# Optimization experiments

Hardware: AMD Instinct MI355X
Metric: run time of the kernel (lower is better)

## Reference

```python
import jax, jax.numpy as jnp
import numpy as np

B, T, NMELS = 2, 2048, 64
D, H, DH, M, L = 256, 4, 64, 384, 4
FF2 = 2 * 4 * D  # GLU doubles the 4*dim hidden


def _layernorm(x, g, b):
    m = x.mean(-1, keepdims=True)
    v = ((x - m) ** 2).mean(-1, keepdims=True)
    return (x - m) * jax.lax.rsqrt(v + 1e-5) * g + b


def _conv(h, w, groups=1, pad='VALID'):
    return jax.lax.conv_general_dilated(h, w, (1, 1), pad, feature_group_count=groups,
                                        dimension_numbers=('NCHW', 'OIHW', 'NCHW'))


def _bn(h, g, b, m, v):
    return (h - m[:, None, None]) * jax.lax.rsqrt(v[:, None, None] + 1e-5) * g[:, None, None] + b[:, None, None]


def setup_inputs():
    key = jax.random.key(0)
    ks = jax.random.split(key, 40)
    def n(i, shape, s):
        return (jax.random.normal(ks[i], shape) * s).astype(jnp.float32)
    z = lambda shape: jnp.zeros(shape, jnp.float32)
    o = lambda shape: jnp.ones(shape, jnp.float32)
    return dict(
        x=n(0, (B, T, NMELS), 1.0),
        conv0_w=n(1, (4, 1, 1, 1), 0.5),
        dw1_w=n(2, (4, 1, 3, 3), 0.3), dw1_b=z(4),
        pw1_w=n(3, (D // 2, 4, 1, 1), 0.5), pw1_b=z(D // 2),
        bn1_g=o(D // 2), bn1_b=z(D // 2), bn1_m=n(4, (D // 2,), 0.05), bn1_v=o(D // 2),
        dw2_w=n(5, (D // 2, 1, 3, 3), 0.3), dw2_b=z(D // 2),
        pw2_w=n(6, (D, D // 2, 1, 1), 0.1), pw2_b=z(D),
        bn2_g=o(D), bn2_b=z(D), bn2_m=n(7, (D,), 0.05), bn2_v=o(D),
        proj_w=n(8, (D, D), 0.06), proj_b=z(D),
        ln0_g=o(D), ln0_b=z(D),
        pos_emb=n(9, (1, T, D), 0.02),
        ln1_g=o((L, D)), ln1_b=z((L, D)),
        wq=n(10, (L, D, D), 0.06), bq=z((L, D)),
        wk=n(11, (L, D, D), 0.06), bk=z((L, D)),
        wv=n(12, (L, D, D), 0.06), bv=z((L, D)),
        wo=n(13, (L, D, D), 0.06), bo=z((L, D)),
        proj_mat=n(14, (L, M, DH), 1.0),
        ln2_g=o((L, D)), ln2_b=z((L, D)),
        ffw1=n(15, (L, D, FF2), 0.06), ffb1=z((L, FF2)),
        ffw2=n(16, (L, FF2 // 2, D), 0.03), ffb2=z((L, D)),
        clf_w1=n(17, (D, D // 2), 0.06), clf_b1=z(D // 2),
        clf_ln_g=o(D // 2), clf_ln_b=z(D // 2),
        clf_w2=n(18, (D // 2, 1), 0.09), clf_b2=z(1),
    )


def reference(x, conv0_w, dw1_w, dw1_b, pw1_w, pw1_b, bn1_g, bn1_b, bn1_m, bn1_v,
              dw2_w, dw2_b, pw2_w, pw2_b, bn2_g, bn2_b, bn2_m, bn2_v,
              proj_w, proj_b, ln0_g, ln0_b, pos_emb,
              ln1_g, ln1_b, wq, bq, wk, bk, wv, bv, wo, bo, proj_mat,
              ln2_g, ln2_b, ffw1, ffb1, ffw2, ffb2,
              clf_w1, clf_b1, clf_ln_g, clf_ln_b, clf_w2, clf_b2):
    pad1 = ((1, 1), (1, 1))
    # conv frontend: [B,T,n_mels] -> [B,1,n_mels,T]
    h = x.transpose(0, 2, 1)[:, None]
    h = _conv(h, conv0_w)
    h = _conv(h, dw1_w, groups=4, pad=pad1) + dw1_b[:, None, None]
    h = _conv(h, pw1_w) + pw1_b[:, None, None]
    h = jax.nn.relu(_bn(h, bn1_g, bn1_b, bn1_m, bn1_v))
    h = _conv(h, dw2_w, groups=D // 2, pad=pad1) + dw2_b[:, None, None]
    h = _conv(h, pw2_w) + pw2_b[:, None, None]
    h = jax.nn.relu(_bn(h, bn2_g, bn2_b, bn2_m, bn2_v))
    h = h.mean(axis=2).transpose(0, 2, 1)  # [B,T,D]
    h = h @ proj_w + proj_b
    h = _layernorm(h, ln0_g, ln0_b) + pos_emb[:, :h.shape[1]]
    # reversible Performer: streams x1 (attn) / x2 (ff), combined by sum
    x1, x2 = h, h
    dn = DH ** -0.25
    for l in range(L):
        a = _layernorm(x2, ln1_g[l], ln1_b[l])
        Bsz, N, _ = a.shape
        q = (a @ wq[l] + bq[l]).reshape(Bsz, N, H, DH).transpose(0, 2, 1, 3)
        k = (a @ wk[l] + bk[l]).reshape(Bsz, N, H, DH).transpose(0, 2, 1, 3)
        v = (a @ wv[l] + bv[l]).reshape(Bsz, N, H, DH).transpose(0, 2, 1, 3)
        # FAVOR+ generalized (ReLU) kernel feature maps, eps=1e-3
        qf = jax.nn.relu(jnp.einsum('bhnd,jd->bhnj', dn * q, proj_mat[l])) + 1e-3
        kf = jax.nn.relu(jnp.einsum('bhnd,jd->bhnj', dn * k, proj_mat[l])) + 1e-3
        d_inv = 1.0 / jnp.einsum('bhnj,bhj->bhn', qf, kf.sum(axis=2))
        ctx = jnp.einsum('bhnj,bhnd->bhjd', kf, v)
        o = jnp.einsum('bhjd,bhnj,bhn->bhnd', ctx, qf, d_inv)
        o = o.transpose(0, 2, 1, 3).reshape(Bsz, N, D)
        x1 = x1 + (o @ wo[l] + bo[l])
        f = _layernorm(x1, ln2_g[l], ln2_b[l])
        u1, u2 = jnp.split(f @ ffw1[l] + ffb1[l], 2, axis=-1)
        x2 = x2 + (jax.nn.gelu(u1, approximate=False) * u2) @ ffw2[l] + ffb2[l]
    h = x1 + x2
    c = jax.nn.relu(_layernorm(h @ clf_w1 + clf_b1, clf_ln_g, clf_ln_b))
    return (c @ clf_w2 + clf_b2)[..., 0]
```

## Files before the change

### kernel.cpp

```cpp
#include <hip/hip_runtime.h>
#include <hip/hip_bf16.h>
#include <math.h>

using bf16 = __hip_bfloat16;
typedef __attribute__((ext_vector_type(8))) short short8;
typedef __attribute__((ext_vector_type(4))) float f32x4;

__device__ __forceinline__ float tof(float x) { return x; }
__device__ __forceinline__ float tof(bf16 x) { return __bfloat162float(x); }
__device__ __forceinline__ float b2f(unsigned short u) {
  union { float f; unsigned int i; } c; c.i = ((unsigned int)u) << 16; return c.f;
}
__device__ __forceinline__ unsigned short f2bu(float v) {
  bf16 h = __float2bfloat16(v);
  return *(unsigned short*)&h;
}
__device__ __forceinline__ void sto1(float* p, float v) { *p = v; }
__device__ __forceinline__ void sto1(bf16* p, float v) { *p = __float2bfloat16(v); }

__device__ __forceinline__ float gelu_exact(float x) {
  return 0.5f * x * (1.f + erff(x * 0.70710678118654752f));
}

__device__ __forceinline__ void llds16(const bf16* g, short* l) {
  __builtin_amdgcn_global_load_lds((const __attribute__((address_space(1))) void*)g,
                                   (__attribute__((address_space(3))) void*)l, 16, 0, 0);
}

__global__ __launch_bounds__(256) void pack_qkv_kernel(
    const float* __restrict__ wq, const float* __restrict__ wk,
    const float* __restrict__ wv, bf16* __restrict__ out)
{
  int idx = blockIdx.x * 256 + threadIdx.x;
  int k = idx & 255;
  int nl = idx >> 8;
  int n = nl % 768, l = nl / 768;
  const float* src = (n < 256) ? wq : (n < 512 ? wk : wv);
  out[idx] = __float2bfloat16(src[(long)l * 65536 + k * 256 + (n & 255)]);
}

__global__ __launch_bounds__(256) void pack_qkvbias_kernel(
    const float* __restrict__ bq, const float* __restrict__ bk,
    const float* __restrict__ bv, float* __restrict__ out)
{
  int i = blockIdx.x * 256 + threadIdx.x;
  if (i >= 3072) return;
  int n = i % 768, l = i / 768;
  const float* src = (n < 256) ? bq : (n < 512 ? bk : bv);
  out[i] = src[l * 256 + (n & 255)];
}

__global__ __launch_bounds__(256) void tconv_kernel(
    const float* __restrict__ in, bf16* __restrict__ out,
    int K, int N, long sin, long sout)
{
  int l = blockIdx.z;
  int idx = blockIdx.x * 256 + threadIdx.x;
  int k = idx % K, n = idx / K;
  out[l * sout + idx] = __float2bfloat16(in[l * sin + (long)k * N + n]);
}

__global__ __launch_bounds__(256) void f2b_kernel(
    const float* __restrict__ in, bf16* __restrict__ out, int n)
{
  int i = blockIdx.x * 256 + threadIdx.x;
  if (i < n) out[i] = __float2bfloat16(in[i]);
}

__global__ __launch_bounds__(256) void zero4_kernel(float* __restrict__ p) {
  int i = (blockIdx.x * 256 + threadIdx.x) * 4;
  float4 z; z.x = 0.f; z.y = 0.f; z.z = 0.f; z.w = 0.f;
  *(float4*)&p[i] = z;
}

__global__ __launch_bounds__(256) void sumb_kernel(
    const float* __restrict__ a, const float* __restrict__ b, bf16* __restrict__ o)
{
  int i = (blockIdx.x * 256 + threadIdx.x) * 4;
  float4 x = *(const float4*)&a[i];
  float4 y = *(const float4*)&b[i];
  ushort4 p;
  p.x = f2bu(x.x + y.x); p.y = f2bu(x.y + y.y);
  p.z = f2bu(x.z + y.z); p.w = f2bu(x.w + y.w);
  *(ushort4*)((unsigned short*)o + i) = p;
}

__global__ __launch_bounds__(256) void front1_kernel(
    const float* __restrict__ x, const float* __restrict__ c0w,
    const float* __restrict__ d1w, const float* __restrict__ d1b,
    const float* __restrict__ p1w, const float* __restrict__ p1b,
    const float* __restrict__ g1, const float* __restrict__ b1,
    const float* __restrict__ m1, const float* __restrict__ v1,
    bf16* __restrict__ A1)
{
  __shared__ float sd[256];
  __shared__ float spw[512];
  __shared__ float ss[128], st[128], sb[128];
  int tid = threadIdx.x;
  int bt = blockIdx.x;
  int b = bt >> 11, t = bt & 2047;
  if (tid < 128) {
    float s = g1[tid] * rsqrtf(v1[tid] + 1e-5f);
    ss[tid] = s;
    st[tid] = b1[tid] - m1[tid] * s;
    sb[tid] = p1b[tid];
#pragma unroll
    for (int c = 0; c < 4; ++c) spw[c * 128 + tid] = p1w[tid * 4 + c];
  }
  {
    int c = tid >> 6, f = tid & 63;
    float cw = c0w[c];
    float acc = d1b[c];
#pragma unroll
    for (int kh = 0; kh < 3; ++kh) {
      int fi = f + kh - 1;
      if (fi < 0 || fi >= 64) continue;
#pragma unroll
      for (int kw = 0; kw < 3; ++kw) {
        int ti = t + kw - 1;
        if (ti < 0 || ti >= 2048) continue;
        acc += d1w[c * 9 + kh * 3 + kw] * cw * x[((long)b * 2048 + ti) * 64 + fi];
      }
    }
    sd[c * 64 + f] = acc;
  }
  __syncthreads();
  long ob = (long)bt * 8192;
  for (int it = 0; it < 32; ++it) {
    int o = it * 256 + tid;
    int f = o >> 7, ci = o & 127;
    float pre = sb[ci];
#pragma unroll
    for (int c = 0; c < 4; ++c) pre = fmaf(spw[c * 128 + ci], sd[c * 64 + f], pre);
    A1[ob + o] = __float2bfloat16(fmaxf(fmaf(ss[ci], pre, st[ci]), 0.f));
  }
}

__global__ __launch_bounds__(256, 4) void convtail_kernel(
    const bf16* __restrict__ A1, const float* __restrict__ w,
    const float* __restrict__ wb, const bf16* __restrict__ w2b,
    const float* __restrict__ pb, const float* __restrict__ g2,
    const float* __restrict__ b2, const float* __restrict__ m2,
    const float* __restrict__ v2, bf16* __restrict__ hconvb)
{
  __shared__ short dw2s[64 * 136];
  __shared__ short Bs[64 * 136];
  __shared__ float red[1024];
  __shared__ float ssc[64], ssh[64];
  int tid = threadIdx.x;
  int lane = tid & 63, wv = tid >> 6;
  int quad = lane >> 4, l15 = lane & 15;
  int rw = (wv >> 1) * 32, cw = (wv & 1) * 32;
  int bt = blockIdx.x, b = bt >> 11, t = bt & 2047;
  int ci8 = (tid & 15) * 8;
  float wreg[9][8], breg[8];
#pragma unroll
  for (int c = 0; c < 8; ++c) {
    breg[c] = wb[ci8 + c];
#pragma unroll
    for (int kk = 0; kk < 9; ++kk) wreg[kk][c] = w[(ci8 + c) * 9 + kk];
  }
  const unsigned short* A1u = (const unsigned short*)A1;
  for (int pass = 0; pass < 4; ++pass) {
    int f = pass * 16 + (tid >> 4);
    float a[8];
#pragma unroll
    for (int c = 0; c < 8; ++c) a[c] = breg[c];
#pragma unroll
    for (int kh = 0; kh < 3; ++kh) {
      int fi = f + kh - 1;
      if (fi < 0 || fi >= 64) continue;
#pragma unroll
      for (int kw = 0; kw < 3; ++kw) {
        int ti = t + kw - 1;
        if (ti < 0 || ti >= 2048) continue;
        short8 u = *(const short8*)&A1u[(((long)b * 2048 + ti) * 64 + fi) * 128 + ci8];
        int kk = kh * 3 + kw;
#pragma unroll
        for (int c = 0; c < 8; ++c)
          a[c] = fmaf(wreg[kk][c], b2f((unsigned short)u[c]), a[c]);
      }
    }
    short8 p;
#pragma unroll
    for (int c = 0; c < 8; ++c) p[c] = (short)f2bu(a[c]);
    *(short8*)&dw2s[f * 136 + ci8] = p;
  }
  for (int ct = 0; ct < 4; ++ct) {
    int co0 = ct * 64;
    __syncthreads();
    for (int l2 = 0; l2 < 4; ++l2) {
      int idx = l2 * 256 + tid;
      int row = idx >> 4, koff = (idx & 15) * 8;
      *(short8*)&Bs[row * 136 + koff] =
          *(const short8*)&w2b[(long)(co0 + row) * 128 + koff];
    }
    if (tid < 64) {
      int co = co0 + tid;
      float s = g2[co] * rsqrtf(v2[co] + 1e-5f);
      ssc[tid] = s;
      ssh[tid] = b2[co] - m2[co] * s + s * pb[co];
    }
    __syncthreads();
    f32x4 zv = {0.f, 0.f, 0.f, 0.f};
    f32x4 acc[2][2] = {{zv, zv}, {zv, zv}};
#pragma unroll
    for (int kc = 0; kc < 4; ++kc) {
      short8 a0 = *(const short8*)&dw2s[(rw + l15) * 136 + kc * 32 + quad * 8];
      short8 a1 = *(const short8*)&dw2s[(rw + 16 + l15) * 136 + kc * 32 + quad * 8];
      short8 b0 = *(const short8*)&Bs[(cw + l15) * 136 + kc * 32 + quad * 8];
      short8 b1 = *(const short8*)&Bs[(cw + 16 + l15) * 136 + kc * 32 + quad * 8];
      acc[0][0] = __builtin_amdgcn_mfma_f32_16x16x32_bf16(a0, b0, acc[0][0], 0, 0, 0);
      acc[0][1] = __builtin_amdgcn_mfma_f32_16x16x32_bf16(a0, b1, acc[0][1], 0, 0, 0);
      acc[1][0] = __builtin_amdgcn_mfma_f32_16x16x32_bf16(a1, b0, acc[1][0], 0, 0, 0);
      acc[1][1] = __builtin_amdgcn_mfma_f32_16x16x32_bf16(a1, b1, acc[1][1], 0, 0, 0);
    }
#pragma unroll
    for (int mi = 0; mi < 2; ++mi)
#pragma unroll
      for (int nj = 0; nj < 2; ++nj) {
        int colg = cw + nj * 16 + l15;
        float s = ssc[colg], sh = ssh[colg];
        float sum = 0.f;
#pragma unroll
        for (int r = 0; r < 4; ++r) sum += fmaxf(fmaf(s, acc[mi][nj][r], sh), 0.f);
        int rowgroup = (wv >> 1) * 8 + mi * 4 + quad;
        red[rowgroup * 64 + colg] = sum;
      }
    __syncthreads();
    if (tid < 64) {
      float s = 0.f;
#pragma unroll
      for (int r = 0; r < 16; ++r) s += red[r * 64 + tid];
      hconvb[(long)bt * 256 + co0 + tid] = __float2bfloat16(s * (1.f / 64.f));
    }
  }
}

__global__ __launch_bounds__(256) void favor_kernel(
    const bf16* __restrict__ qkvb, const bf16* __restrict__ pm,
    bf16* __restrict__ qf, bf16* __restrict__ kfT, float dn)
{
  __shared__ short As[4096];
  __shared__ short Bs[4096];
  int tid = threadIdx.x;
  int lane = tid & 63, w = tid >> 6;
  int quad = lane >> 4, l15 = lane & 15;
  int rw = (w >> 1) * 32, cw = (w & 1) * 32;
  int r0 = blockIdx.x * 64, n0 = blockIdx.y * 64;
  int z16 = blockIdx.z;
  bool isK = z16 >= 8;
  int z = z16 & 7, zb = z >> 2, zh = z & 3;
  const bf16* A = qkvb + (isK ? 256 : 0) + (long)zb * 1572864 + zh * 64;
  f32x4 zv = {0.f, 0.f, 0.f, 0.f};
  f32x4 acc[2][2] = {{zv, zv}, {zv, zv}};
  const bf16* Ag = A + (long)(r0 + (tid >> 2)) * 768 + ((tid & 3) * 8);
  const bf16* Bg = pm + (long)(n0 + (tid >> 2)) * 64 + ((tid & 3) * 8);
  llds16(Ag, &As[tid * 8]);
  llds16(Ag + 32, &As[tid * 8 + 2048]);
  llds16(Bg, &Bs[tid * 8]);
  llds16(Bg + 32, &Bs[tid * 8 + 2048]);
  __syncthreads();
#pragma unroll
  for (int c = 0; c < 2; ++c) {
    short8 a0 = *(const short8*)&As[c * 2048 + (rw + l15) * 32 + quad * 8];
    short8 a1 = *(const short8*)&As[c * 2048 + (rw + 16 + l15) * 32 + quad * 8];
    short8 b0 = *(const short8*)&Bs[c * 2048 + (cw + l15) * 32 + quad * 8];
    short8 b1 = *(const short8*)&Bs[c * 2048 + (cw + 16 + l15) * 32 + quad * 8];
    acc[0][0] = __builtin_amdgcn_mfma_f32_16x16x32_bf16(a0, b0, acc[0][0], 0, 0, 0);
    acc[0][1] = __builtin_amdgcn_mfma_f32_16x16x32_bf16(a0, b1, acc[0][1], 0, 0, 0);
    acc[1][0] = __builtin_amdgcn_mfma_f32_16x16x32_bf16(a1, b0, acc[1][0], 0, 0, 0);
    acc[1][1] = __builtin_amdgcn_mfma_f32_16x16x32_bf16(a1, b1, acc[1][1], 0, 0, 0);
  }
  bf16* qfz = qf + (long)zb * 3145728 + (long)zh * 786432;
  unsigned short* kfz = (unsigned short*)kfT + (long)zb * 3145728 + (long)zh * 786432;
#pragma unroll
  for (int mi = 0; mi < 2; ++mi)
#pragma unroll
    for (int nj = 0; nj < 2; ++nj) {
      int colg = n0 + cw + nj * 16 + l15;
      int rbase = r0 + rw + mi * 16 + quad * 4;
      float ov[4];
#pragma unroll
      for (int r = 0; r < 4; ++r)
        ov[r] = fmaxf(acc[mi][nj][r] * dn, 0.f) + 1e-3f;
      if (!isK) {
#pragma unroll
        for (int r = 0; r < 4; ++r)
          qfz[(long)(rbase + r) * 384 + colg] = __float2bfloat16(ov[r]);
      } else {
        ushort4 p;
        p.x = f2bu(ov[0]); p.y = f2bu(ov[1]); p.z = f2bu(ov[2]); p.w = f2bu(ov[3]);
        *(ushort4*)&kfz[(long)colg * 2048 + rbase] = p;
      }
    }
}

__global__ __launch_bounds__(256) void rowsum_kernel(
    const bf16* __restrict__ kfT, float* __restrict__ ksum)
{
  int z = blockIdx.x;
  int j = blockIdx.y * 4 + (threadIdx.x >> 6);
  int lane = threadIdx.x & 63;
  const short* base = (const short*)kfT + ((long)z * 384 + j) * 2048;
  float acc = 0.f;
#pragma unroll
  for (int i = 0; i < 4; ++i) {
    short8 v = *(const short8*)&base[i * 512 + lane * 8];
#pragma unroll
    for (int e = 0; e < 8; ++e) acc += b2f((unsigned short)v[e]);
  }
#pragma unroll
  for (int o = 32; o > 0; o >>= 1) acc += __shfl_xor(acc, o, 64);
  if (lane == 0) ksum[z * 384 + j] = acc;
}

template <typename CTy, int EPI>
__global__ __launch_bounds__(256) void mgemm_kernel(
    const bf16* __restrict__ A, const bf16* __restrict__ Bt,
    const float* __restrict__ bias, const float* __restrict__ res,
    const float* __restrict__ rowsc, CTy* __restrict__ C, bf16* __restrict__ C2,
    int K, int lda, int ldbt, int ldc,
    long sAb, long sAh, long sBb, long sBh, long sCb, long sCh,
    long sRb, long sRh, int Hdiv, float alpha)
{
  __shared__ short As[4096];
  __shared__ short Bs[4096];
  __shared__ short Bs2[(EPI == 8) ? 4096 : 8];
  int tid = threadIdx.x;
  int lane = tid & 63, w = tid >> 6;
  int quad = lane >> 4, l15 = lane & 15;
  int rw = (w >> 1) * 32, cw = (w & 1) * 32;
  int r0 = blockIdx.x * 64, n0 = blockIdx.y * 64;
  int zb = blockIdx.z / Hdiv, zh = blockIdx.z % Hdiv;
  A += zb * sAb + zh * sAh;
  Bt += zb * sBb + zh * sBh;
  C += zb * sCb + zh * sCh;
  if (res) res += zb * sCb + zh * sCh;
  const float* rsp = (EPI == 3) ? rowsc + zb * sRb + zh * sRh : nullptr;
  f32x4 zv = {0.f, 0.f, 0.f, 0.f};
  f32x4 acc[2][2] = {{zv, zv}, {zv, zv}};
  f32x4 acc2[2][2] = {{zv, zv}, {zv, zv}};
  const bf16* Ag = A + (long)(r0 + (tid >> 2)) * lda + ((tid & 3) * 8);
  const bf16* Bg = Bt + (long)(n0 + (tid >> 2)) * ldbt + ((tid & 3) * 8);
  const bf16* Bg2 = (EPI == 8) ? Bg + sRb : nullptr;
  short* Asd = &As[tid * 8];
  short* Bsd = &Bs[tid * 8];
  short* Bs2d = &Bs2[(EPI == 8) ? tid * 8 : 0];
  for (int k0 = 0; k0 < K; k0 += 64) {
    if (k0) __syncthreads();
    llds16(Ag + k0, Asd);
    llds16(Ag + k0 + 32, Asd + 2048);
    llds16(Bg + k0, Bsd);
    llds16(Bg + k0 + 32, Bsd + 2048);
    if constexpr (EPI == 8) {
      llds16(Bg2 + k0, Bs2d);
      llds16(Bg2 + k0 + 32, Bs2d + 2048);
    }
    __syncthreads();
#pragma unroll
    for (int c = 0; c < 2; ++c) {
      short8 a0 = *(const short8*)&As[c * 2048 + (rw + l15) * 32 + quad * 8];
      short8 a1 = *(const short8*)&As[c * 2048 + (rw + 16 + l15) * 32 + quad * 8];
      short8 b0 = *(const short8*)&Bs[c * 2048 + (cw + l15) * 32 + quad * 8];
      short8 b1 = *(const short8*)&Bs[c * 2048 + (cw + 16 + l15) * 32 + quad * 8];
      acc[0][0] = __builtin_amdgcn_mfma_f32_16x16x32_bf16(a0, b0, acc[0][0], 0, 0, 0);
      acc[0][1] = __builtin_amdgcn_mfma_f32_16x16x32_bf16(a0, b1, acc[0][1], 0, 0, 0);
      acc[1][0] = __builtin_amdgcn_mfma_f32_16x16x32_bf16(a1, b0, acc[1][0], 0, 0, 0);
      acc[1][1] = __builtin_amdgcn_mfma_f32_16x16x32_bf16(a1, b1, acc[1][1], 0, 0, 0);
      if constexpr (EPI == 8) {
        short8 c0 = *(const short8*)&Bs2[c * 2048 + (cw + l15) * 32 + quad * 8];
        short8 c1 = *(const short8*)&Bs2[c * 2048 + (cw + 16 + l15) * 32 + quad * 8];
        acc2[0][0] = __builtin_amdgcn_mfma_f32_16x16x32_bf16(a0, c0, acc2[0][0], 0, 0, 0);
        acc2[0][1] = __builtin_amdgcn_mfma_f32_16x16x32_bf16(a0, c1, acc2[0][1], 0, 0, 0);
        acc2[1][0] = __builtin_amdgcn_mfma_f32_16x16x32_bf16(a1, c0, acc2[1][0], 0, 0, 0);
        acc2[1][1] = __builtin_amdgcn_mfma_f32_16x16x32_bf16(a1, c1, acc2[1][1], 0, 0, 0);
      }
    }
  }
#pragma unroll
  for (int mi = 0; mi < 2; ++mi)
#pragma unroll
    for (int nj = 0; nj < 2; ++nj) {
      int colg = n0 + cw + nj * 16 + l15;
      float bv_ = bias ? bias[colg] : 0.f;
      float bv2 = (EPI == 8) ? bias[colg + 1024] : 0.f;
      int rbase = r0 + rw + mi * 16 + quad * 4;
      float ov[4];
#pragma unroll
      for (int r = 0; r < 4; ++r) {
        float v = acc[mi][nj][r];
        if constexpr (EPI == 0 || EPI == 5) {
          v += bv_;
        } else if constexpr (EPI == 1) {
          v += bv_ + res[(long)(rbase + r) * ldc + colg];
        } else if constexpr (EPI == 3) {
          v *= rsp[rbase + r];
        } else if constexpr (EPI == 8) {
          v = gelu_exact(v + bv_) * (acc2[mi][nj][r] + bv2);
        }
        ov[r] = v;
      }
      if constexpr (EPI == 5) {
        if (colg < 512) {
#pragma unroll
          for (int r = 0; r < 4; ++r) sto1(&C[(long)(rbase + r) * ldc + colg], ov[r]);
        } else {
          int bb = rbase >> 11, t0 = rbase & 2047;
          long off = (((long)bb * 4 + ((colg - 512) >> 6)) * 64 + (colg & 63)) * 2048 + t0;
          ushort4 p;
          p.x = f2bu(ov[0]); p.y = f2bu(ov[1]); p.z = f2bu(ov[2]); p.w = f2bu(ov[3]);
          *(ushort4*)((unsigned short*)C2 + off) = p;
        }
      } else if constexpr (EPI == 7) {
#pragma unroll
        for (int r = 0; r < 4; ++r)
          atomicAdd((float*)&C[(long)(rbase + r) * ldc + colg], ov[r]);
      } else {
#pragma unroll
        for (int r = 0; r < 4; ++r) sto1(&C[(long)(rbase + r) * ldc + colg], ov[r]);
      }
    }
  (void)alpha;
}

template <int DIM, bool RELU, bool ADDPOS, bool DUAL, typename OTy>
__global__ __launch_bounds__(256) void ln_kernel(
    const float* __restrict__ in, const float* __restrict__ g,
    const float* __restrict__ b, const float* __restrict__ pos,
    OTy* __restrict__ out0, float* __restrict__ out1)
{
  constexpr int CH = DIM / 64;
  int row = blockIdx.x * 4 + (threadIdx.x >> 6);
  int lane = threadIdx.x & 63;
  const float* rp = in + (long)row * DIM + lane * CH;
  float v[CH];
#pragma unroll
  for (int i = 0; i < CH; ++i) v[i] = rp[i];
  float s = 0.f;
#pragma unroll
  for (int i = 0; i < CH; ++i) s += v[i];
#pragma unroll
  for (int o = 32; o > 0; o >>= 1) s += __shfl_xor(s, o, 64);
  float mean = s * (1.f / DIM);
  float q = 0.f;
#pragma unroll
  for (int i = 0; i < CH; ++i) { float d = v[i] - mean; q += d * d; }
#pragma unroll
  for (int o = 32; o > 0; o >>= 1) q += __shfl_xor(q, o, 64);
  float rstd = rsqrtf(q * (1.f / DIM) + 1e-5f);
  int t = row & 2047;
#pragma unroll
  for (int i = 0; i < CH; ++i) {
    int c = lane * CH + i;
    float o = (v[i] - mean) * rstd * g[c] + b[c];
    if constexpr (ADDPOS) o += pos[(long)t * DIM + c];
    if constexpr (RELU) o = fmaxf(o, 0.f);
    sto1(&out0[(long)row * DIM + c], o);
    if constexpr (DUAL) out1[(long)row * DIM + c] = o;
  }
}

__global__ __launch_bounds__(256) void dinv_kernel(
    const bf16* __restrict__ qf, const float* __restrict__ ksum,
    float* __restrict__ dinv)
{
  int z = blockIdx.x;
  int t = blockIdx.y * 4 + (threadIdx.x >> 6);
  int lane = threadIdx.x & 63;
  const bf16* qr = qf + ((long)z * 2048 + t) * 384;
  const float* ks = ksum + z * 384;
  float acc = 0.f;
#pragma unroll
  for (int i = 0; i < 6; ++i) {
    int j = lane + i * 64;
    acc = fmaf(tof(qr[j]), ks[j], acc);
  }
#pragma unroll
  for (int o = 32; o > 0; o >>= 1) acc += __shfl_xor(acc, o, 64);
  if (lane == 0) dinv[z * 2048 + t] = 1.f / acc;
}

__global__ __launch_bounds__(256) void clf2_kernel(
    const float* __restrict__ c2, const float* __restrict__ w,
    const float* __restrict__ b, float* __restrict__ out)
{
  int row = blockIdx.x * 4 + (threadIdx.x >> 6);
  int lane = threadIdx.x & 63;
  const float* rp = c2 + (long)row * 128 + lane * 2;
  float acc = rp[0] * w[lane * 2] + rp[1] * w[lane * 2 + 1];
#pragma unroll
  for (int o = 32; o > 0; o >>= 1) acc += __shfl_xor(acc, o, 64);
  if (lane == 0) out[row] = acc + b[0];
}

extern "C" void kernel_launch(void* const* d_in, const int* in_sizes, int n_in,
                              void* d_out, int out_size, void* d_ws, size_t ws_size,
                              hipStream_t stream)
{
  const float* X    = (const float*)d_in[0];
  const float* c0w  = (const float*)d_in[1];
  const float* d1w  = (const float*)d_in[2];
  const float* d1b  = (const float*)d_in[3];
  const float* p1w  = (const float*)d_in[4];
  const float* p1b  = (const float*)d_in[5];
  const float* g1   = (const float*)d_in[6];
  const float* b1   = (const float*)d_in[7];
  const float* m1   = (const float*)d_in[8];
  const float* v1   = (const float*)d_in[9];
  const float* d2w  = (const float*)d_in[10];
  const float* d2b  = (const float*)d_in[11];
  const float* p2w  = (const float*)d_in[12];
  const float* p2b  = (const float*)d_in[13];
  const float* g2   = (const float*)d_in[14];
  const float* b2   = (const float*)d_in[15];
  const float* m2   = (const float*)d_in[16];
  const float* v2   = (const float*)d_in[17];
  const float* projw= (const float*)d_in[18];
  const float* projb= (const float*)d_in[19];
  const float* ln0g = (const float*)d_in[20];
  const float* ln0b = (const float*)d_in[21];
  const float* pos  = (const float*)d_in[22];
  const float* ln1g = (const float*)d_in[23];
  const float* ln1b = (const float*)d_in[24];
  const float* wq   = (const float*)d_in[25];
  const float* bq   = (const float*)d_in[26];
  const float* wk   = (const float*)d_in[27];
  const float* bk   = (const float*)d_in[28];
  const float* wv   = (const float*)d_in[29];
  const float* bv   = (const float*)d_in[30];
  const float* wo   = (const float*)d_in[31];
  const float* bo   = (const float*)d_in[32];
  const float* pmat = (const float*)d_in[33];
  const float* ln2g = (const float*)d_in[34];
  const float* ln2b = (const float*)d_in[35];
  const float* ffw1 = (const float*)d_in[36];
  const float* ffb1 = (const float*)d_in[37];
  const float* ffw2 = (const float*)d_in[38];
  const float* ffb2 = (const float*)d_in[39];
  const float* cw1  = (const float*)d_in[40];
  const float* cb1  = (const float*)d_in[41];
  const float* clng = (const float*)d_in[42];
  const float* clnb = (const float*)d_in[43];
  const float* cw2  = (const float*)d_in[44];
  const float* cb2  = (const float*)d_in[45];
  (void)in_sizes; (void)n_in; (void)out_size; (void)ws_size;

  float* ws     = (float*)d_ws;
  float* x1     = ws;
  float* x2     = ws + 1048576;
  float* lnb32  = ws + 2097152;
  bf16*  lnb16  = (bf16*)(ws + 3145728);
  bf16*  hconvb = (bf16*)(ws + 3407872);
  bf16*  obufb  = (bf16*)(ws + 3670016);
  bf16*  qkvb   = (bf16*)(ws + 3932160);
  bf16*  vT     = (bf16*)(ws + 5505024);
  bf16*  qf     = (bf16*)(ws + 6029312);
  bf16*  kfT    = (bf16*)(ws + 9175040);
  float* ctx32  = ws + 12320768;
  float* ksum   = ws + 12517376;
  float* dinvp  = ws + 12521472;
  bf16*  ctxb   = (bf16*)(ws + 12537856);
  float* c1     = ws + 12587008;
  float* c2     = ws + 13111296;
  bf16*  gb2    = (bf16*)(ws + 16633856);
  bf16*  A1     = (bf16*)(ws + 3670016);
  bf16*  wqkv_bf= (bf16*)(ws + 20447232);
  float* qkvbias= ws + 20840448;
  bf16*  f1w_bf = (bf16*)(ws + 20843520);
  bf16*  f2w_bf = (bf16*)(ws + 21892096);
  bf16*  wo_bf  = (bf16*)(ws + 22416384);
  bf16*  pm_bf  = (bf16*)(ws + 22547456);
  bf16*  projwT = (bf16*)(ws + 22596608);
  bf16*  cw1T   = (bf16*)(ws + 22629376);
  bf16*  pw2_bf = (bf16*)(ws + 22645760);
  bf16*  sbuf   = qkvb;

  const float dn = 0.35355339059327378f;

  pack_qkv_kernel<<<3072, 256, 0, stream>>>(wq, wk, wv, wqkv_bf);
  pack_qkvbias_kernel<<<12, 256, 0, stream>>>(bq, bk, bv, qkvbias);
  tconv_kernel<<<dim3(2048, 1, 4), 256, 0, stream>>>(ffw1, f1w_bf, 256, 2048, 524288, 524288);
  tconv_kernel<<<dim3(1024, 1, 4), 256, 0, stream>>>(ffw2, f2w_bf, 1024, 256, 262144, 262144);
  tconv_kernel<<<dim3(256, 1, 4), 256, 0, stream>>>(wo, wo_bf, 256, 256, 65536, 65536);
  tconv_kernel<<<dim3(256, 1, 1), 256, 0, stream>>>(projw, projwT, 256, 256, 65536, 65536);
  tconv_kernel<<<dim3(128, 1, 1), 256, 0, stream>>>(cw1, cw1T, 256, 128, 32768, 32768);
  f2b_kernel<<<384, 256, 0, stream>>>(pmat, pm_bf, 98304);
  f2b_kernel<<<128, 256, 0, stream>>>(p2w, pw2_bf, 32768);

  front1_kernel<<<4096, 256, 0, stream>>>(X, c0w, d1w, d1b, p1w, p1b, g1, b1, m1, v1, A1);
  convtail_kernel<<<4096, 256, 0, stream>>>(A1, d2w, d2b, pw2_bf, p2b, g2, b2, m2, v2, hconvb);

  mgemm_kernel<float, 0><<<dim3(64, 4, 1), 256, 0, stream>>>(
      hconvb, projwT, projb, nullptr, nullptr, lnb32, nullptr,
      256, 256, 256, 256, 0, 0, 0, 0, 0, 0, 0, 0, 1, 1.f);
  ln_kernel<256, false, true, true, float><<<1024, 256, 0, stream>>>(
      lnb32, ln0g, ln0b, pos, x1, x2);

  for (int l = 0; l < 4; ++l) {
    const bf16* wqkv_l = wqkv_bf + (size_t)l * 196608;
    const float* qb_l  = qkvbias + l * 768;
    const bf16* pm_l   = pm_bf + (size_t)l * 24576;
    const bf16* wo_l   = wo_bf + (size_t)l * 65536;
    const float* bov   = bo + l * 256;
    const bf16* f1w_l  = f1w_bf + (size_t)l * 524288;
    const float* f1b_l = ffb1 + l * 2048;
    const bf16* f2w_l  = f2w_bf + (size_t)l * 262144;
    const float* f2b_l = ffb2 + l * 256;

    ln_kernel<256, false, false, false, bf16><<<1024, 256, 0, stream>>>(
        x2, ln1g + l * 256, ln1b + l * 256, nullptr, lnb16, nullptr);
    mgemm_kernel<bf16, 5><<<dim3(64, 12, 1), 256, 0, stream>>>(
        lnb16, wqkv_l, qb_l, nullptr, nullptr, qkvb, vT,
        256, 256, 256, 768, 0, 0, 0, 0, 0, 0, 0, 0, 1, 1.f);
    zero4_kernel<<<192, 256, 0, stream>>>(ctx32);
    favor_kernel<<<dim3(32, 6, 16), 256, 0, stream>>>(
        qkvb, pm_l, qf, kfT, dn);
    rowsum_kernel<<<dim3(8, 96), 256, 0, stream>>>(kfT, ksum);
    dinv_kernel<<<dim3(8, 512), 256, 0, stream>>>(qf, ksum, dinvp);
    mgemm_kernel<float, 7><<<dim3(1, 6, 64), 256, 0, stream>>>(
        vT, kfT, nullptr, nullptr, nullptr, ctx32, nullptr,
        256, 2048, 2048, 384, 131072, 256, 786432, 256, 24576, 0, 0, 0, 8, 1.f);
    f2b_kernel<<<768, 256, 0, stream>>>(ctx32, ctxb, 196608);
    mgemm_kernel<bf16, 3><<<dim3(32, 1, 8), 256, 0, stream>>>(
        qf, ctxb, nullptr, nullptr, dinvp, obufb, nullptr,
        384, 384, 384, 256, 3145728, 786432, 98304, 24576, 524288, 64, 8192, 2048, 4, 1.f);
    mgemm_kernel<float, 1><<<dim3(64, 4, 1), 256, 0, stream>>>(
        obufb, wo_l, bov, x1, nullptr, x1, nullptr,
        256, 256, 256, 256, 0, 0, 0, 0, 0, 0, 0, 0, 1, 1.f);
    ln_kernel<256, false, false, false, bf16><<<1024, 256, 0, stream>>>(
        x1, ln2g + l * 256, ln2b + l * 256, nullptr, lnb16, nullptr);
    mgemm_kernel<bf16, 8><<<dim3(64, 16, 1), 256, 0, stream>>>(
        lnb16, f1w_l, f1b_l, nullptr, nullptr, gb2, nullptr,
        256, 256, 256, 1024, 0, 0, 0, 0, 0, 0, 262144, 0, 1, 1.f);
    mgemm_kernel<float, 1><<<dim3(64, 4, 1), 256, 0, stream>>>(
        gb2, f2w_l, f2b_l, x2, nullptr, x2, nullptr,
        1024, 1024, 1024, 256, 0, 0, 0, 0, 0, 0, 0, 0, 1, 1.f);
  }

  sumb_kernel<<<1024, 256, 0, stream>>>(x1, x2, sbuf);
  mgemm_kernel<float, 0><<<dim3(64, 2, 1), 256, 0, stream>>>(
      sbuf, cw1T, cb1, nullptr, nullptr, c1, nullptr,
      256, 256, 256, 128, 0, 0, 0, 0, 0, 0, 0, 0, 1, 1.f);
  ln_kernel<128, true, false, false, float><<<1024, 256, 0, stream>>>(
      c1, clng, clnb, nullptr, c2, nullptr);
  clf2_kernel<<<1024, 256, 0, stream>>>(c2, cw2, cb2, (float*)d_out);
}
```

Baseline: 640.5 us.

## Split-K FF2 GEMM with atomics, fuse ctx zeroing, retune convtail loads

The FF2 down-projection GEMM is split along K into two halves that atomically accumulate into x2, adding the bias only on the first split, so the launch has more blocks. Zeroing of the context accumulator moves into the rowsum kernel, removing one launch. The convtail kernel stores depthwise weights in bf16 registers, batches all nine input loads before the FMAs, and stages the pointwise weights with a direct-to-LDS helper into an unpadded layout. Risks include more atomic traffic, LDS bank conflicts from dropping the padding, and slightly lower precision from rounding the depthwise weights to bf16.

```diff
diff --git a/kernel.cpp b/kernel.cpp
--- a/kernel.cpp
+++ b/kernel.cpp
@@ -65,12 +65,6 @@
 {
   int i = blockIdx.x * 256 + threadIdx.x;
   if (i < n) out[i] = __float2bfloat16(in[i]);
-}
-
-__global__ __launch_bounds__(256) void zero4_kernel(float* __restrict__ p) {
-  int i = (blockIdx.x * 256 + threadIdx.x) * 4;
-  float4 z; z.x = 0.f; z.y = 0.f; z.z = 0.f; z.w = 0.f;
-  *(float4*)&p[i] = z;
 }
 
 __global__ __launch_bounds__(256) void sumb_kernel(
@@ -144,7 +138,7 @@
     const float* __restrict__ v2, bf16* __restrict__ hconvb)
 {
   __shared__ short dw2s[64 * 136];
-  __shared__ short Bs[64 * 136];
+  __shared__ short Bs[8192];
   __shared__ float red[1024];
   __shared__ float ssc[64], ssh[64];
   int tid = threadIdx.x;
@@ -153,34 +147,45 @@
   int rw = (wv >> 1) * 32, cw = (wv & 1) * 32;
   int bt = blockIdx.x, b = bt >> 11, t = bt & 2047;
   int ci8 = (tid & 15) * 8;
-  float wreg[9][8], breg[8];
-#pragma unroll
-  for (int c = 0; c < 8; ++c) {
-    breg[c] = wb[ci8 + c];
-#pragma unroll
-    for (int kk = 0; kk < 9; ++kk) wreg[kk][c] = w[(ci8 + c) * 9 + kk];
+  short8 wregh[9];
+  float breg[8];
+#pragma unroll
+  for (int c = 0; c < 8; ++c) breg[c] = wb[ci8 + c];
+#pragma unroll
+  for (int kk = 0; kk < 9; ++kk) {
+    short8 wv8;
+#pragma unroll
+    for (int c = 0; c < 8; ++c) wv8[c] = (short)f2bu(w[(ci8 + c) * 9 + kk]);
+    wregh[kk] = wv8;
   }
   const unsigned short* A1u = (const unsigned short*)A1;
   for (int pass = 0; pass < 4; ++pass) {
     int f = pass * 16 + (tid >> 4);
-    float a[8];
-#pragma unroll
-    for (int c = 0; c < 8; ++c) a[c] = breg[c];
+    short8 u[9];
 #pragma unroll
     for (int kh = 0; kh < 3; ++kh) {
       int fi = f + kh - 1;
-      if (fi < 0 || fi >= 64) continue;
 #pragma unroll
       for (int kw = 0; kw < 3; ++kw) {
         int ti = t + kw - 1;
-        if (ti < 0 || ti >= 2048) continue;
-        short8 u = *(const short8*)&A1u[(((long)b * 2048 + ti) * 64 + fi) * 128 + ci8];
         int kk = kh * 3 + kw;
-#pragma unroll
-        for (int c = 0; c < 8; ++c)
-          a[c] = fmaf(wreg[kk][c], b2f((unsigned short)u[c]), a[c]);
+        if (fi >= 0 && fi < 64 && ti >= 0 && ti < 2048) {
+          u[kk] = *(const short8*)&A1u[(((long)b * 2048 + ti) * 64 + fi) * 128 + ci8];
+        } else {
+          short8 z = {0, 0, 0, 0, 0, 0, 0, 0};
+          u[kk] = z;
+        }
       }
     }
+    float a[8];
+#pragma unroll
+    for (int c = 0; c < 8; ++c) a[c] = breg[c];
+#pragma unroll
+    for (int kk = 0; kk < 9; ++kk)
+#pragma unroll
+      for (int c = 0; c < 8; ++c)
+        a[c] = fmaf(b2f((unsigned short)wregh[kk][c]),
+                    b2f((unsigned short)u[kk][c]), a[c]);
     short8 p;
 #pragma unroll
     for (int c = 0; c < 8; ++c) p[c] = (short)f2bu(a[c]);
@@ -189,12 +194,10 @@
   for (int ct = 0; ct < 4; ++ct) {
     int co0 = ct * 64;
     __syncthreads();
-    for (int l2 = 0; l2 < 4; ++l2) {
-      int idx = l2 * 256 + tid;
-      int row = idx >> 4, koff = (idx & 15) * 8;
-      *(short8*)&Bs[row * 136 + koff] =
-          *(const short8*)&w2b[(long)(co0 + row) * 128 + koff];
-    }
+#pragma unroll
+    for (int c = 0; c < 4; ++c)
+      llds16(w2b + (long)(co0 + c * 16 + (tid >> 4)) * 128 + (tid & 15) * 8,
+             &Bs[c * 2048 + tid * 8]);
     if (tid < 64) {
       int co = co0 + tid;
       float s = g2[co] * rsqrtf(v2[co] + 1e-5f);
@@ -208,8 +211,8 @@
     for (int kc = 0; kc < 4; ++kc) {
       short8 a0 = *(const short8*)&dw2s[(rw + l15) * 136 + kc * 32 + quad * 8];
       short8 a1 = *(const short8*)&dw2s[(rw + 16 + l15) * 136 + kc * 32 + quad * 8];
-      short8 b0 = *(const short8*)&Bs[(cw + l15) * 136 + kc * 32 + quad * 8];
-      short8 b1 = *(const short8*)&Bs[(cw + 16 + l15) * 136 + kc * 32 + quad * 8];
+      short8 b0 = *(const short8*)&Bs[(cw + l15) * 128 + kc * 32 + quad * 8];
+      short8 b1 = *(const short8*)&Bs[(cw + 16 + l15) * 128 + kc * 32 + quad * 8];
       acc[0][0] = __builtin_amdgcn_mfma_f32_16x16x32_bf16(a0, b0, acc[0][0], 0, 0, 0);
       acc[0][1] = __builtin_amdgcn_mfma_f32_16x16x32_bf16(a0, b1, acc[0][1], 0, 0, 0);
       acc[1][0] = __builtin_amdgcn_mfma_f32_16x16x32_bf16(a1, b0, acc[1][0], 0, 0, 0);
@@ -297,8 +300,14 @@
 }
 
 __global__ __launch_bounds__(256) void rowsum_kernel(
-    const bf16* __restrict__ kfT, float* __restrict__ ksum)
-{
+    const bf16* __restrict__ kfT, float* __restrict__ ksum,
+    float* __restrict__ ctx32)
+{
+  int flat = (blockIdx.x * 96 + blockIdx.y) * 256 + threadIdx.x;
+  if (flat < 49152) {
+    float4 zq; zq.x = 0.f; zq.y = 0.f; zq.z = 0.f; zq.w = 0.f;
+    *(float4*)&ctx32[flat * 4] = zq;
+  }
   int z = blockIdx.x;
   int j = blockIdx.y * 4 + (threadIdx.x >> 6);
   int lane = threadIdx.x & 63;
@@ -398,6 +407,8 @@
           v *= rsp[rbase + r];
         } else if constexpr (EPI == 8) {
           v = gelu_exact(v + bv_) * (acc2[mi][nj][r] + bv2);
+        } else if constexpr (EPI == 9) {
+          v += (zh == 0) ? bv_ : 0.f;
         }
         ov[r] = v;
       }
@@ -412,7 +423,7 @@
           p.x = f2bu(ov[0]); p.y = f2bu(ov[1]); p.z = f2bu(ov[2]); p.w = f2bu(ov[3]);
           *(ushort4*)((unsigned short*)C2 + off) = p;
         }
-      } else if constexpr (EPI == 7) {
+      } else if constexpr (EPI == 7 || EPI == 9) {
 #pragma unroll
         for (int r = 0; r < 4; ++r)
           atomicAdd((float*)&C[(long)(rbase + r) * ldc + colg], ov[r]);
@@ -613,10 +624,9 @@
     mgemm_kernel<bf16, 5><<<dim3(64, 12, 1), 256, 0, stream>>>(
         lnb16, wqkv_l, qb_l, nullptr, nullptr, qkvb, vT,
         256, 256, 256, 768, 0, 0, 0, 0, 0, 0, 0, 0, 1, 1.f);
-    zero4_kernel<<<192, 256, 0, stream>>>(ctx32);
     favor_kernel<<<dim3(32, 6, 16), 256, 0, stream>>>(
         qkvb, pm_l, qf, kfT, dn);
-    rowsum_kernel<<<dim3(8, 96), 256, 0, stream>>>(kfT, ksum);
+    rowsum_kernel<<<dim3(8, 96), 256, 0, stream>>>(kfT, ksum, ctx32);
     dinv_kernel<<<dim3(8, 512), 256, 0, stream>>>(qf, ksum, dinvp);
     mgemm_kernel<float, 7><<<dim3(1, 6, 64), 256, 0, stream>>>(
         vT, kfT, nullptr, nullptr, nullptr, ctx32, nullptr,
@@ -633,9 +643,9 @@
     mgemm_kernel<bf16, 8><<<dim3(64, 16, 1), 256, 0, stream>>>(
         lnb16, f1w_l, f1b_l, nullptr, nullptr, gb2, nullptr,
         256, 256, 256, 1024, 0, 0, 0, 0, 0, 0, 262144, 0, 1, 1.f);
-    mgemm_kernel<float, 1><<<dim3(64, 4, 1), 256, 0, stream>>>(
-        gb2, f2w_l, f2b_l, x2, nullptr, x2, nullptr,
-        1024, 1024, 1024, 256, 0, 0, 0, 0, 0, 0, 0, 0, 1, 1.f);
+    mgemm_kernel<float, 9><<<dim3(64, 4, 2), 256, 0, stream>>>(
+        gb2, f2w_l, f2b_l, nullptr, nullptr, x2, nullptr,
+        512, 1024, 1024, 256, 0, 512, 0, 512, 0, 0, 0, 0, 2, 1.f);
   }
 
   sumb_kernel<<<1024, 256, 0, stream>>>(x1, x2, sbuf);
```

Result: no change. 647.1 us (+1.0%).
